# Kernel tuning notes

Hardware: AMD Instinct MI355X
Metric: run time of the kernel (lower is better)

Reference implementation:

```python
import jax, jax.numpy as jnp
import numpy as np

N, D_IN, D_H, D_OUT, E = 32768, 1024, 2048, 1024, 8

def setup_inputs() -> dict:
    key = jax.random.key(0)
    ks = jax.random.split(key, 8)
    s_in = 1.0 / np.sqrt(D_IN)
    s_h = 1.0 / np.sqrt(D_H)
    return {
        "x": jax.random.normal(ks[0], (N, D_IN), dtype=jnp.float32),
        "Wr": jax.random.normal(ks[1], (D_IN, E), dtype=jnp.float32) * s_in,
        "br": jnp.zeros((E,), dtype=jnp.float32),
        "W1": jax.random.normal(ks[2], (E, D_IN, D_H), dtype=jnp.float32) * s_in,
        "b1": jnp.zeros((E, D_H), dtype=jnp.float32),
        "W2": jax.random.normal(ks[3], (E, D_H, D_OUT), dtype=jnp.float32) * s_h,
        "b2": jnp.zeros((E, D_OUT), dtype=jnp.float32),
    }

def reference(x, Wr, br, W1, b1, W2, b2):
    # Supervised router: encoder is Identity, router is Linear + softmax.
    router_probs = jax.nn.softmax(x @ Wr + br, axis=-1)            # [N, E]
    router_probs_max = jnp.max(router_probs, axis=-1)              # [N]
    routes = jnp.argmax(router_probs, axis=-1)                     # [N] int
    counts = jnp.sum(jax.nn.one_hot(routes, E, dtype=x.dtype), axis=0)  # [E]

    # Top-1 dispatch: each token goes through exactly one expert MLP.
    # Small fixed loop over experts (E=8); mask-combine replaces gather/scatter.
    out = jnp.zeros((N, D_OUT), dtype=x.dtype)
    for e in range(E):
        h = jax.nn.relu(x @ W1[e] + b1[e])                         # [N, D_H]
        y = h @ W2[e] + b2[e]                                      # [N, D_OUT]
        out = out + jnp.where((routes == e)[:, None], y, jnp.zeros((), x.dtype))
    # Straight-through scaling: value 1 in fwd, routes grad through router prob.
    scale = router_probs_max / jax.lax.stop_gradient(router_probs_max)
    out = out * scale[:, None]
    return out, router_probs, counts
```

## Files before the change

kernel.cpp:

```cpp
#include <hip/hip_runtime.h>
#include <stdint.h>


#define NTOK   32768
#define DIN    1024
#define DH     2048
#define DOUT   1024
#define NEXP   8

typedef unsigned short u16;
typedef __bf16 bf16x8 __attribute__((ext_vector_type(8)));
typedef float  f32x4  __attribute__((ext_vector_type(4)));
typedef const __attribute__((address_space(1))) void gvoid_t;
typedef __attribute__((address_space(3))) void svoid_t;

__device__ __forceinline__ u16 f2bf(float f) {
  union { float f; uint32_t u; } v; v.f = f;
  return (u16)((v.u + 0x7FFFu + ((v.u >> 16) & 1u)) >> 16);
}

__global__ __launch_bounds__(256) void k_router(
    const float* __restrict__ x, const float* __restrict__ Wr,
    const float* __restrict__ br, float* __restrict__ probs,
    int* __restrict__ routes)
{
  __shared__ float wr_s[NEXP * DIN];
  int tid = threadIdx.x;
  for (int idx = tid; idx < DIN * NEXP / 4; idx += 256) {
    float4 v = ((const float4*)Wr)[idx];
    int k = idx >> 1, r = (idx & 1) * 4;
    wr_s[(r + 0) * DIN + k] = v.x;
    wr_s[(r + 1) * DIN + k] = v.y;
    wr_s[(r + 2) * DIN + k] = v.z;
    wr_s[(r + 3) * DIN + k] = v.w;
  }
  __syncthreads();
  int lane = tid & 63, wv = tid >> 6;
  int t = blockIdx.x * 4 + wv;
  const float* xr = x + (size_t)t * DIN;
  float acc[NEXP];
  #pragma unroll
  for (int e = 0; e < NEXP; ++e) acc[e] = 0.f;
  #pragma unroll
  for (int i = 0; i < 4; ++i) {
    int k = i * 256 + lane * 4;
    float4 xv = *(const float4*)(xr + k);
    #pragma unroll
    for (int e = 0; e < NEXP; ++e) {
      float4 w4 = *(const float4*)(wr_s + e * DIN + k);
      acc[e] += xv.x * w4.x + xv.y * w4.y + xv.z * w4.z + xv.w * w4.w;
    }
  }
  #pragma unroll
  for (int off = 32; off >= 1; off >>= 1) {
    #pragma unroll
    for (int e = 0; e < NEXP; ++e) acc[e] += __shfl_xor(acc[e], off, 64);
  }
  if (lane == 0) {
    float l[NEXP], m = -1e30f;
    #pragma unroll
    for (int e = 0; e < NEXP; ++e) { l[e] = acc[e] + br[e]; m = fmaxf(m, l[e]); }
    float p[NEXP], s = 0.f;
    #pragma unroll
    for (int e = 0; e < NEXP; ++e) { p[e] = expf(l[e] - m); s += p[e]; }
    float inv = 1.f / s;
    int am = 0; float best = l[0];
    #pragma unroll
    for (int e = 1; e < NEXP; ++e) if (l[e] > best) { best = l[e]; am = e; }
    #pragma unroll
    for (int e = 0; e < NEXP; ++e) probs[(size_t)t * NEXP + e] = p[e] * inv;
    routes[t] = am;
  }
}

__global__ __launch_bounds__(256) void k_count(
    const int* __restrict__ routes, int* __restrict__ aux)
{
  int t = blockIdx.x * 256 + threadIdx.x;
  int e = routes[t];
  int lane = threadIdx.x & 63;
  #pragma unroll
  for (int ee = 0; ee < NEXP; ++ee) {
    unsigned long long m = __ballot(e == ee);
    if (lane == 0 && m) atomicAdd(&aux[ee], (int)__popcll(m));
  }
}

__global__ void k_prefix(int* __restrict__ aux, float* __restrict__ counts_out)
{
  if (threadIdx.x == 0) {
    int off = 0, nt = 0;
    for (int e = 0; e < NEXP; ++e) {
      int c = aux[e];
      counts_out[e] = (float)c;
      aux[24 + e] = off;
      int tiles = (c + 127) >> 7;
      for (int tt = 0; tt < tiles; ++tt) {
        aux[128 + nt] = e;
        aux[512 + nt] = off + tt * 128;
        aux[896 + nt] = off + c;
        ++nt;
      }
      off += c;
    }
    aux[16] = nt;
  }
}

__global__ __launch_bounds__(256) void k_assign(
    const int* __restrict__ routes, int* __restrict__ aux,
    int* __restrict__ pos_of_tok, int* __restrict__ tok_of_pos)
{
  int t = blockIdx.x * 256 + threadIdx.x;
  int e = routes[t];
  int lane = threadIdx.x & 63;
  int p = 0;
  #pragma unroll
  for (int ee = 0; ee < NEXP; ++ee) {
    unsigned long long m = __ballot(e == ee);
    int base = 0;
    if (lane == 0 && m) base = atomicAdd(&aux[8 + ee], (int)__popcll(m));
    base = __shfl(base, 0, 64);
    if (e == ee)
      p = aux[24 + ee] + base + (int)__popcll(m & ((1ull << lane) - 1ull));
  }
  pos_of_tok[t] = p;
  tok_of_pos[p] = t;
}

__global__ __launch_bounds__(256) void k_permute(
    const float* __restrict__ x, const int* __restrict__ pos_of_tok,
    u16* __restrict__ xs)
{
  int t = blockIdx.x * 2 + (threadIdx.x >> 7);
  int j = threadIdx.x & 127;
  int p = pos_of_tok[t];
  const float4* src = (const float4*)(x + (size_t)t * DIN);
  u16* dst = xs + (size_t)p * DIN;
  #pragma unroll
  for (int h = 0; h < 2; ++h) {
    float4 v = src[h * 128 + j];
    ushort4 o;
    o.x = f2bf(v.x); o.y = f2bf(v.y); o.z = f2bf(v.z); o.w = f2bf(v.w);
    *(ushort4*)(dst + (h * 128 + j) * 4) = o;
  }
}

__global__ __launch_bounds__(256) void k_transpose(
    const float* __restrict__ src, u16* __restrict__ dst, int K, int Nn)
{
  __shared__ float tile[64][65];
  int e = blockIdx.z;
  int k0 = blockIdx.x * 64, n0 = blockIdx.y * 64;
  const float* s = src + ((size_t)e * K + k0) * Nn + n0;
  int r = threadIdx.x >> 6, c = threadIdx.x & 63;
  #pragma unroll
  for (int i = 0; i < 16; ++i)
    tile[r + i * 4][c] = s[(size_t)(r + i * 4) * Nn + c];
  __syncthreads();
  u16* d = dst + ((size_t)e * Nn + n0) * K + k0;
  #pragma unroll
  for (int i = 0; i < 16; ++i) {
    int nr = r + i * 4;
    d[(size_t)nr * K + c] = f2bf(tile[c][nr]);
  }
}

template<int MODE>
__global__ __launch_bounds__(256, 4) void k_gemm(
    const u16* __restrict__ A, const u16* __restrict__ Bt,
    const float* __restrict__ bias, u16* __restrict__ Hout,
    float* __restrict__ Yout, const int* __restrict__ tok_of_pos,
    const int* __restrict__ aux, int K, int Nn, int nbyl)
{
  int nwg = gridDim.x;
  int bid = blockIdx.x;
  int wg  = (bid & 7) * (nwg >> 3) + (bid >> 3);
  int by  = wg & ((1 << nbyl) - 1);
  int bx  = wg >> nbyl;
  if (bx >= aux[16]) return;
  int e  = aux[128 + bx];
  int r0 = aux[512 + bx];
  int r1 = aux[896 + bx];
  int bn0 = by << 7;

  __shared__ __align__(16) u16 As[128 * 64];
  __shared__ __align__(16) u16 Bs[128 * 64];

  int tid = threadIdx.x;
  int lane = tid & 63, wv = tid >> 6;
  int wr = wv >> 1, wc = wv & 1;
  const u16* Be = Bt + (size_t)e * Nn * K;

  auto stage = [&](int kt) {
    int k0 = kt * 64;
    #pragma unroll
    for (int r = 0; r < 4; ++r) {
      int L = (r * 256 + tid) * 16;
      int row = L >> 7;
      int sl = ((L >> 4) & 7) ^ (row & 7);
      int grow = r0 + row; grow = grow < NTOK ? grow : NTOK - 1;
      __builtin_amdgcn_global_load_lds(
          (gvoid_t*)((const char*)(A + (size_t)grow * K + k0) + sl * 16),
          (svoid_t*)((char*)As + L), 16, 0, 0);
    }
    #pragma unroll
    for (int r = 0; r < 4; ++r) {
      int L = (r * 256 + tid) * 16;
      int row = L >> 7;
      int sl = ((L >> 4) & 7) ^ (row & 7);
      __builtin_amdgcn_global_load_lds(
          (gvoid_t*)((const char*)(Be + (size_t)(bn0 + row) * K + k0) + sl * 16),
          (svoid_t*)((char*)Bs + L), 16, 0, 0);
    }
  };

  f32x4 acc[4][4];
  #pragma unroll
  for (int i = 0; i < 4; ++i)
    #pragma unroll
    for (int j = 0; j < 4; ++j)
      acc[i][j] = (f32x4){0.f, 0.f, 0.f, 0.f};

  int KT = K >> 6;
  stage(0);
  for (int kt = 0; kt < KT; ++kt) {
    __syncthreads();
    const char* As_c = (const char*)As;
    const char* Bs_c = (const char*)Bs;
    #pragma unroll
    for (int kk = 0; kk < 2; ++kk) {
      int sw = ((kk * 4 + (lane >> 4)) ^ (lane & 7)) << 4;
      bf16x8 a[4], b[4];
      #pragma unroll
      for (int f = 0; f < 4; ++f)
        a[f] = *(const bf16x8*)(As_c + (wr * 64 + f * 16 + (lane & 15)) * 128 + sw);
      #pragma unroll
      for (int f = 0; f < 4; ++f)
        b[f] = *(const bf16x8*)(Bs_c + (wc * 64 + f * 16 + (lane & 15)) * 128 + sw);
      #pragma unroll
      for (int i = 0; i < 4; ++i)
        #pragma unroll
        for (int j = 0; j < 4; ++j)
          acc[i][j] = __builtin_amdgcn_mfma_f32_16x16x32_bf16(a[i], b[j], acc[i][j], 0, 0, 0);
    }
    __syncthreads();
    if (kt + 1 < KT) stage(kt + 1);
  }

  const float* be = bias + (size_t)e * Nn;
  float bv[4];
  #pragma unroll
  for (int j = 0; j < 4; ++j) bv[j] = be[bn0 + wc * 64 + j * 16 + (lane & 15)];
  #pragma unroll
  for (int i = 0; i < 4; ++i) {
    #pragma unroll
    for (int q = 0; q < 4; ++q) {
      int r = r0 + wr * 64 + i * 16 + (lane >> 4) * 4 + q;
      if (r < r1) {
        if (MODE == 0) {
          u16* dst = Hout + (size_t)r * Nn + bn0 + wc * 64 + (lane & 15);
          #pragma unroll
          for (int j = 0; j < 4; ++j)
            dst[j * 16] = f2bf(fmaxf(acc[i][j][q] + bv[j], 0.f));
        } else {
          int tok = tok_of_pos[r];
          float* dst = Yout + (size_t)tok * Nn + bn0 + wc * 64 + (lane & 15);
          #pragma unroll
          for (int j = 0; j < 4; ++j)
            dst[j * 16] = acc[i][j][q] + bv[j];
        }
      }
    }
  }
}

extern "C" void kernel_launch(void* const* d_in, const int* in_sizes, int n_in,
                              void* d_out, int out_size, void* d_ws, size_t ws_size,
                              hipStream_t stream)
{
  const float* x  = (const float*)d_in[0];
  const float* Wr = (const float*)d_in[1];
  const float* br = (const float*)d_in[2];
  const float* W1 = (const float*)d_in[3];
  const float* b1 = (const float*)d_in[4];
  const float* W2 = (const float*)d_in[5];
  const float* b2 = (const float*)d_in[6];

  float* out    = (float*)d_out;
  float* probs  = out + (size_t)NTOK * DOUT;
  float* counts = probs + (size_t)NTOK * NEXP;

  char* ws = (char*)d_ws;
  u16* xs          = (u16*)(ws);
  u16* h           = (u16*)(ws + 67108864);
  u16* W1t         = (u16*)(ws + 201326592);
  u16* W2t         = (u16*)(ws + 234881024);
  int* aux         = (int*)(ws + 268435456);
  int* routes      = (int*)(ws + 268451840);
  int* pos_of_tok  = (int*)(ws + 268582912);
  int* tok_of_pos  = (int*)(ws + 268713984);

  (void)hipMemsetAsync(aux, 0, 16384, stream);
  k_router<<<NTOK / 4, 256, 0, stream>>>(x, Wr, br, probs, routes);
  k_count<<<NTOK / 256, 256, 0, stream>>>(routes, aux);
  k_transpose<<<dim3(DIN / 64, DH / 64, NEXP), 256, 0, stream>>>(W1, W1t, DIN, DH);
  k_transpose<<<dim3(DH / 64, DOUT / 64, NEXP), 256, 0, stream>>>(W2, W2t, DH, DOUT);
  k_prefix<<<1, 64, 0, stream>>>(aux, counts);
  k_assign<<<NTOK / 256, 256, 0, stream>>>(routes, aux, pos_of_tok, tok_of_pos);
  k_permute<<<NTOK / 2, 256, 0, stream>>>(x, pos_of_tok, xs);
  k_gemm<0><<<264 * 16, 256, 0, stream>>>(xs, W1t, b1, h, nullptr, nullptr, aux, DIN, DH, 4);
  k_gemm<1><<<264 * 8, 256, 0, stream>>>(h, W2t, b2, nullptr, out, tok_of_pos, aux, DH, DOUT, 3);
}
```

Measured before the change: 553.6 us.

## Fuse bf16 cast into router, gather rows in GEMM1, merge transposes, parallelize prefix

The router kernel now writes a bf16 copy of x in token order, which removes the separate permute kernel. The first GEMM gathers A rows through tok_of_pos when staging into LDS. The two weight transposes become one launch, and the prefix kernel fills its tile tables with many threads instead of one. This removes one full pass over x and a few launches, at the cost of less contiguous gathered loads in GEMM1.

```diff
diff --git a/kernel.cpp b/kernel.cpp
--- a/kernel.cpp
+++ b/kernel.cpp
@@ -22,7 +22,7 @@
 __global__ __launch_bounds__(256) void k_router(
     const float* __restrict__ x, const float* __restrict__ Wr,
     const float* __restrict__ br, float* __restrict__ probs,
-    int* __restrict__ routes)
+    int* __restrict__ routes, u16* __restrict__ xb)
 {
   __shared__ float wr_s[NEXP * DIN];
   int tid = threadIdx.x;
@@ -38,6 +38,7 @@
   int lane = tid & 63, wv = tid >> 6;
   int t = blockIdx.x * 4 + wv;
   const float* xr = x + (size_t)t * DIN;
+  u16* xbrow = xb + (size_t)t * DIN;
   float acc[NEXP];
   #pragma unroll
   for (int e = 0; e < NEXP; ++e) acc[e] = 0.f;
@@ -45,6 +46,9 @@
   for (int i = 0; i < 4; ++i) {
     int k = i * 256 + lane * 4;
     float4 xv = *(const float4*)(xr + k);
+    ushort4 o;
+    o.x = f2bf(xv.x); o.y = f2bf(xv.y); o.z = f2bf(xv.z); o.w = f2bf(xv.w);
+    *(ushort4*)(xbrow + k) = o;
     #pragma unroll
     for (int e = 0; e < NEXP; ++e) {
       float4 w4 = *(const float4*)(wr_s + e * DIN + k);
@@ -86,24 +90,32 @@
   }
 }
 
-__global__ void k_prefix(int* __restrict__ aux, float* __restrict__ counts_out)
-{
-  if (threadIdx.x == 0) {
-    int off = 0, nt = 0;
+__global__ __launch_bounds__(256) void k_prefix(int* __restrict__ aux, float* __restrict__ counts_out)
+{
+  __shared__ int s_off[NEXP], s_cnt[NEXP], s_tb[NEXP], s_nt;
+  int tid = threadIdx.x;
+  if (tid == 0) {
+    int off = 0, tb = 0;
     for (int e = 0; e < NEXP; ++e) {
       int c = aux[e];
       counts_out[e] = (float)c;
+      s_cnt[e] = c; s_off[e] = off; s_tb[e] = tb;
       aux[24 + e] = off;
-      int tiles = (c + 127) >> 7;
-      for (int tt = 0; tt < tiles; ++tt) {
-        aux[128 + nt] = e;
-        aux[512 + nt] = off + tt * 128;
-        aux[896 + nt] = off + c;
-        ++nt;
-      }
-      off += c;
-    }
-    aux[16] = nt;
+      off += c; tb += (c + 127) >> 7;
+    }
+    s_nt = tb;
+    aux[16] = tb;
+  }
+  __syncthreads();
+  int nt = s_nt;
+  for (int i = tid; i < nt; i += 256) {
+    int e = 0;
+    #pragma unroll
+    for (int k = 1; k < NEXP; ++k) if (i >= s_tb[k]) e = k;
+    int tt = i - s_tb[e];
+    aux[128 + i] = e;
+    aux[512 + i] = s_off[e] + tt * 128;
+    aux[896 + i] = s_off[e] + s_cnt[e];
   }
 }
 
@@ -128,30 +140,17 @@
   tok_of_pos[p] = t;
 }
 
-__global__ __launch_bounds__(256) void k_permute(
-    const float* __restrict__ x, const int* __restrict__ pos_of_tok,
-    u16* __restrict__ xs)
-{
-  int t = blockIdx.x * 2 + (threadIdx.x >> 7);
-  int j = threadIdx.x & 127;
-  int p = pos_of_tok[t];
-  const float4* src = (const float4*)(x + (size_t)t * DIN);
-  u16* dst = xs + (size_t)p * DIN;
-  #pragma unroll
-  for (int h = 0; h < 2; ++h) {
-    float4 v = src[h * 128 + j];
-    ushort4 o;
-    o.x = f2bf(v.x); o.y = f2bf(v.y); o.z = f2bf(v.z); o.w = f2bf(v.w);
-    *(ushort4*)(dst + (h * 128 + j) * 4) = o;
-  }
-}
-
 __global__ __launch_bounds__(256) void k_transpose(
-    const float* __restrict__ src, u16* __restrict__ dst, int K, int Nn)
-{
+    const float* __restrict__ W1, u16* __restrict__ W1t,
+    const float* __restrict__ W2, u16* __restrict__ W2t)
+{
+  int z = blockIdx.z;
+  const float* src; u16* dst; int K, Nn, e;
+  if (z < NEXP) { src = W1; dst = W1t; K = DIN; Nn = DH;   e = z; }
+  else          { src = W2; dst = W2t; K = DH;  Nn = DOUT; e = z - NEXP; }
+  int k0 = blockIdx.x * 64, n0 = blockIdx.y * 64;
+  if (k0 >= K || n0 >= Nn) return;
   __shared__ float tile[64][65];
-  int e = blockIdx.z;
-  int k0 = blockIdx.x * 64, n0 = blockIdx.y * 64;
   const float* s = src + ((size_t)e * K + k0) * Nn + n0;
   int r = threadIdx.x >> 6, c = threadIdx.x & 63;
   #pragma unroll
@@ -166,7 +165,7 @@
   }
 }
 
-template<int MODE>
+template<int MODE, int GATHER>
 __global__ __launch_bounds__(256, 4) void k_gemm(
     const u16* __restrict__ A, const u16* __restrict__ Bt,
     const float* __restrict__ bias, u16* __restrict__ Hout,
@@ -192,16 +191,22 @@
   int wr = wv >> 1, wc = wv & 1;
   const u16* Be = Bt + (size_t)e * Nn * K;
 
+  int tk[4];
+  #pragma unroll
+  for (int r = 0; r < 4; ++r) {
+    int gr = r0 + r * 32 + (tid >> 3);
+    gr = gr < NTOK ? gr : NTOK - 1;
+    tk[r] = GATHER ? tok_of_pos[gr] : gr;
+  }
+
   auto stage = [&](int kt) {
     int k0 = kt * 64;
     #pragma unroll
     for (int r = 0; r < 4; ++r) {
       int L = (r * 256 + tid) * 16;
-      int row = L >> 7;
-      int sl = ((L >> 4) & 7) ^ (row & 7);
-      int grow = r0 + row; grow = grow < NTOK ? grow : NTOK - 1;
+      int sl = ((L >> 4) & 7) ^ ((L >> 7) & 7);
       __builtin_amdgcn_global_load_lds(
-          (gvoid_t*)((const char*)(A + (size_t)grow * K + k0) + sl * 16),
+          (gvoid_t*)((const char*)(A + (size_t)tk[r] * K + k0) + sl * 16),
           (svoid_t*)((char*)As + L), 16, 0, 0);
     }
     #pragma unroll
@@ -292,7 +297,7 @@
   float* counts = probs + (size_t)NTOK * NEXP;
 
   char* ws = (char*)d_ws;
-  u16* xs          = (u16*)(ws);
+  u16* xb          = (u16*)(ws);
   u16* h           = (u16*)(ws + 67108864);
   u16* W1t         = (u16*)(ws + 201326592);
   u16* W2t         = (u16*)(ws + 234881024);
@@ -302,13 +307,11 @@
   int* tok_of_pos  = (int*)(ws + 268713984);
 
   (void)hipMemsetAsync(aux, 0, 16384, stream);
-  k_router<<<NTOK / 4, 256, 0, stream>>>(x, Wr, br, probs, routes);
+  k_router<<<NTOK / 4, 256, 0, stream>>>(x, Wr, br, probs, routes, xb);
   k_count<<<NTOK / 256, 256, 0, stream>>>(routes, aux);
-  k_transpose<<<dim3(DIN / 64, DH / 64, NEXP), 256, 0, stream>>>(W1, W1t, DIN, DH);
-  k_transpose<<<dim3(DH / 64, DOUT / 64, NEXP), 256, 0, stream>>>(W2, W2t, DH, DOUT);
-  k_prefix<<<1, 64, 0, stream>>>(aux, counts);
+  k_transpose<<<dim3(32, 32, 2 * NEXP), 256, 0, stream>>>(W1, W1t, W2, W2t);
+  k_prefix<<<1, 256, 0, stream>>>(aux, counts);
   k_assign<<<NTOK / 256, 256, 0, stream>>>(routes, aux, pos_of_tok, tok_of_pos);
-  k_permute<<<NTOK / 2, 256, 0, stream>>>(x, pos_of_tok, xs);
-  k_gemm<0><<<264 * 16, 256, 0, stream>>>(xs, W1t, b1, h, nullptr, nullptr, aux, DIN, DH, 4);
-  k_gemm<1><<<264 * 8, 256, 0, stream>>>(h, W2t, b2, nullptr, out, tok_of_pos, aux, DH, DOUT, 3);
-}
+  k_gemm<0, 1><<<264 * 16, 256, 0, stream>>>(xb, W1t, b1, h, nullptr, tok_of_pos, aux, DIN, DH, 4);
+  k_gemm<1, 0><<<264 * 8, 256, 0, stream>>>(h, W2t, b2, nullptr, out, tok_of_pos, aux, DH, DOUT, 3);
+}
```

New measurement: 526.2 us. 5.0% less time.
